# Kernel optimization log

Hardware: AMD Instinct MI355X
Metric: run time of the kernel (lower is better)

## Reference

```python
import jax, jax.numpy as jnp
import numpy as np

DIM = 256

def setup_inputs() -> dict:
    key = jax.random.key(0)
    k1, k2 = jax.random.split(key)
    X = jax.random.normal(k1, (4, 4096, DIM), dtype=jnp.float32)
    # fused QKV projection weight, stored as (dim, 3*dim) so y = X @ W + b
    W = jax.random.normal(k2, (DIM, 3 * DIM), dtype=jnp.float32) * (1.0 / np.sqrt(DIM))
    b = jnp.zeros((3 * DIM,), dtype=jnp.float32)
    return {"X": X, "W": W, "b": b}

def reference(X, W, b):
    dim = X.shape[-1]
    QKV = X @ W + b                      # [B, S, 3*dim]
    Q, K, V = jnp.split(QKV, 3, axis=-1)  # each [B, S, dim]
    scores = jnp.einsum('bqd,bkd->bqk', Q, K) / jnp.sqrt(jnp.float32(dim))
    weights = jax.nn.softmax(scores, axis=-1)  # [B, S, S]
    return jnp.einsum('bqk,bkd->bqd', weights, V)
```

## Files before the change

kernel.cpp:

```cpp
#include <hip/hip_runtime.h>
#include <hip/hip_bf16.h>
#include <hip/hip_fp16.h>

#define DIMD 256
#define SLEN 4096
#define KT 32

typedef __attribute__((ext_vector_type(8))) short short8;
typedef __attribute__((ext_vector_type(4))) short bf16x4;
typedef __attribute__((ext_vector_type(4))) float f32x4;
typedef unsigned int u32;

__device__ __forceinline__ ushort f2bf(float x) {
  union { float f; unsigned u; } v; v.f = x;
  unsigned r = v.u + 0x7fffu + ((v.u >> 16) & 1u);
  return (ushort)(r >> 16);
}

typedef __attribute__((address_space(1))) const u32 g_u32;
typedef __attribute__((address_space(3))) u32 l_u32;
__device__ __forceinline__ void gld_lds16(const void* g, void* l) {
  __builtin_amdgcn_global_load_lds((g_u32*)g, (l_u32*)l, 16, 0, 0);
}

__global__ __launch_bounds__(256) void wt_prep(const float* __restrict__ W,
                                               ushort* __restrict__ Wt) {
  __shared__ float T[32][257];
  const int t = threadIdx.x;
  const int n0 = blockIdx.x * 32;
#pragma unroll
  for (int pass = 0; pass < 8; ++pass) {
    const int k = pass * 32 + (t >> 3);
    const int c4 = (t & 7) * 4;
    const float4 f = *(const float4*)&W[(size_t)k * 768 + n0 + c4];
    T[c4 + 0][k] = f.x; T[c4 + 1][k] = f.y; T[c4 + 2][k] = f.z; T[c4 + 3][k] = f.w;
  }
  __syncthreads();
  const int n = t >> 3, kb = (t & 7) * 32;
#pragma unroll
  for (int j8 = 0; j8 < 4; ++j8) {
    short8 o;
#pragma unroll
    for (int j = 0; j < 8; ++j) o[j] = (short)f2bf(T[n][kb + j8 * 8 + j]);
    *(short8*)&Wt[(size_t)(n0 + n) * 256 + kb + j8 * 8] = o;
  }
}

__global__ __launch_bounds__(256, 2) void qkv_proj(const float* __restrict__ X,
                                                   const ushort* __restrict__ Wt,
                                                   const float* __restrict__ bias,
                                                   ushort* __restrict__ Qo,
                                                   ushort* __restrict__ Ko,
                                                   ushort* __restrict__ Vto) {
  __shared__ ushort Xs[128 * 36];
  __shared__ ushort Ws[256 * 36];
  const int tid = threadIdx.x;
  const int w = tid >> 6, lane = tid & 63;
  const int qa = lane & 15, hi = lane >> 4;
  const int m0 = blockIdx.x * 128;
  const int seg = blockIdx.y;
  const int n0 = seg * 256;

  f32x4 acc[2][16];
#pragma unroll
  for (int t = 0; t < 2; ++t)
#pragma unroll
    for (int dc = 0; dc < 16; ++dc) acc[t][dc] = (f32x4){0.f, 0.f, 0.f, 0.f};

  for (int k0 = 0; k0 < 256; k0 += 32) {
    __syncthreads();
#pragma unroll
    for (int pass = 0; pass < 4; ++pass) {
      const int row = pass * 32 + (tid >> 3);
      const int c = tid & 7;
      const float4 f = *(const float4*)&X[(size_t)(m0 + row) * 256 + k0 + c * 4];
      bf16x4 h = {(short)f2bf(f.x), (short)f2bf(f.y), (short)f2bf(f.z), (short)f2bf(f.w)};
      *(bf16x4*)&Xs[row * 36 + c * 4] = h;
    }
#pragma unroll
    for (int pass = 0; pass < 4; ++pass) {
      const int n = pass * 64 + (tid >> 2);
      const int c = (tid & 3) * 8;
      short8 v = *(const short8*)&Wt[(size_t)(n0 + n) * 256 + k0 + c];
      *(short8*)&Ws[n * 36 + c] = v;
    }
    __syncthreads();
    const short8 xf0 = *(const short8*)&Xs[(w * 32 + qa) * 36 + hi * 8];
    const short8 xf1 = *(const short8*)&Xs[(w * 32 + 16 + qa) * 36 + hi * 8];
    __builtin_amdgcn_s_setprio(1);
#pragma unroll
    for (int dc = 0; dc < 16; ++dc) {
      const short8 wf = *(const short8*)&Ws[(dc * 16 + qa) * 36 + hi * 8];
      acc[0][dc] = __builtin_amdgcn_mfma_f32_16x16x32_bf16(xf0, wf, acc[0][dc], 0, 0, 0);
      acc[1][dc] = __builtin_amdgcn_mfma_f32_16x16x32_bf16(xf1, wf, acc[1][dc], 0, 0, 0);
    }
    __builtin_amdgcn_s_setprio(0);
  }

  const float sc = (seg == 0) ? 0.0625f : 1.0f;
#pragma unroll
  for (int dc = 0; dc < 16; ++dc) {
    const int nn = dc * 16 + qa;
    const float bv = bias[n0 + nn];
#pragma unroll
    for (int t = 0; t < 2; ++t) {
#pragma unroll
      for (int r = 0; r < 4; ++r) {
        const int m = m0 + w * 32 + t * 16 + hi * 4 + r;
        const ushort h = f2bf((acc[t][dc][r] + bv) * sc);
        if (seg == 0)      Qo[(size_t)m * 256 + nn] = h;
        else if (seg == 1) Ko[(size_t)m * 256 + nn] = h;
        else {
          const int bi = m >> 12, s = m & 4095;
          const int sp = (s & ~31) | ((s & 3) | (((s >> 4) & 1) << 2) | (((s >> 2) & 3) << 3));
          Vto[((size_t)bi * 256 + nn) * 4096 + sp] = h;
        }
      }
    }
  }
}

__device__ __forceinline__ void stage_kv(ushort* KsB, ushort* VsB,
                                         const ushort* Kb, const ushort* Vtb,
                                         int kv0, int w, int lane) {
#pragma unroll
  for (int it = 0; it < 2; ++it) {
    const int row = w * 4 + it * 2 + (lane >> 5);
    const int cb = (lane & 31) * 16;
    const char* src = (const char*)Kb + (size_t)(kv0 + row) * 512 + (cb ^ ((row & 7) << 4));
    gld_lds16(src, (char*)KsB + w * 2048 + it * 1024);
  }
#pragma unroll
  for (int it = 0; it < 2; ++it) {
    const int d = w * 32 + it * 16 + (lane >> 2);
    const int cb = (lane & 3) * 16;
    const char* src = (const char*)Vtb + (size_t)d * 8192 + (size_t)kv0 * 2 + (cb ^ ((d & 3) << 4));
    gld_lds16(src, (char*)VsB + w * 2048 + it * 1024);
  }
}

__global__ __launch_bounds__(512, 2) void flash_attn(const ushort* __restrict__ Q,
                                                     const ushort* __restrict__ K,
                                                     const ushort* __restrict__ Vt,
                                                     float* __restrict__ Out,
                                                     __half* __restrict__ Op,
                                                     float* __restrict__ Mp,
                                                     int nsplit, int kvn) {
  __shared__ __attribute__((aligned(16))) ushort Ks[3][KT * DIMD];
  __shared__ __attribute__((aligned(16))) ushort Vs[3][DIMD * KT];

  const int tid = threadIdx.x;
  const int w = tid >> 6, lane = tid & 63;
  const int nwg = gridDim.x;
  const int wg = (blockIdx.x & 7) * (nwg >> 3) + (blockIdx.x >> 3);
  const int split = wg >> 6;
  const int rest = wg & 63;
  const int b = rest >> 4;
  const int q0 = (rest & 15) * 256;
  const int qa = lane & 15, hi = lane >> 4;

  const ushort* Qr0 = Q + (size_t)(b * SLEN + q0 + w * 32 + qa) * DIMD;
  short8 qf0[8], qf1[8];
#pragma unroll
  for (int dc = 0; dc < 8; ++dc) {
    qf0[dc] = *(const short8*)(Qr0 + dc * 32 + hi * 8);
    qf1[dc] = *(const short8*)(Qr0 + 16 * DIMD + dc * 32 + hi * 8);
  }

  const f32x4 zero = {0.f, 0.f, 0.f, 0.f};
  f32x4 acc[2][16];
#pragma unroll
  for (int t = 0; t < 2; ++t)
#pragma unroll
    for (int dc = 0; dc < 16; ++dc) acc[t][dc] = zero;
  float mold0 = -1e30f, lrun0 = 0.f, mold1 = -1e30f, lrun1 = 0.f;
  short8 af0, af1;

  const ushort* Kb = K + (size_t)b * SLEN * DIMD;
  const ushort* Vtb = Vt + (size_t)b * DIMD * SLEN;
  const int kv_begin = split * kvn;
  const int nt = kvn / KT;

  auto QK_SM = [&](const char* KsB) {
    f32x4 sa0 = zero, sa1 = zero, sb0 = zero, sb1 = zero;
    __builtin_amdgcn_s_setprio(1);
#pragma unroll
    for (int dc = 0; dc < 8; ++dc) {
      const int cb = dc * 64 + hi * 16;
      const short8 kf0 = *(const short8*)(KsB + ((qa * 512 + cb) ^ ((qa & 7) << 4)));
      const short8 kf1 = *(const short8*)(KsB + (((qa + 16) * 512 + cb) ^ ((qa & 7) << 4)));
      sa0 = __builtin_amdgcn_mfma_f32_16x16x32_bf16(kf0, qf0[dc], sa0, 0, 0, 0);
      sa1 = __builtin_amdgcn_mfma_f32_16x16x32_bf16(kf1, qf0[dc], sa1, 0, 0, 0);
      sb0 = __builtin_amdgcn_mfma_f32_16x16x32_bf16(kf0, qf1[dc], sb0, 0, 0, 0);
      sb1 = __builtin_amdgcn_mfma_f32_16x16x32_bf16(kf1, qf1[dc], sb1, 0, 0, 0);
    }
    __builtin_amdgcn_s_setprio(0);
    float m8a = fmaxf(fmaxf(fmaxf(sa0[0], sa0[1]), fmaxf(sa0[2], sa0[3])),
                      fmaxf(fmaxf(sa1[0], sa1[1]), fmaxf(sa1[2], sa1[3])));
    float m8b = fmaxf(fmaxf(fmaxf(sb0[0], sb0[1]), fmaxf(sb0[2], sb0[3])),
                      fmaxf(fmaxf(sb1[0], sb1[1]), fmaxf(sb1[2], sb1[3])));
    m8a = fmaxf(m8a, __shfl_xor(m8a, 16)); m8a = fmaxf(m8a, __shfl_xor(m8a, 32));
    m8b = fmaxf(m8b, __shfl_xor(m8b, 16)); m8b = fmaxf(m8b, __shfl_xor(m8b, 32));
    if (!__all(fmaxf(m8a - mold0, m8b - mold1) <= 4.0f)) {
      const float mn0 = fmaxf(mold0, m8a), fr0 = __expf(mold0 - mn0);
      const float mn1 = fmaxf(mold1, m8b), fr1 = __expf(mold1 - mn1);
      mold0 = mn0; lrun0 *= fr0; mold1 = mn1; lrun1 *= fr1;
      float fA[4], fB[4];
#pragma unroll
      for (int r = 0; r < 4; ++r) { fA[r] = __shfl(fr0, hi * 4 + r); fB[r] = __shfl(fr1, hi * 4 + r); }
#pragma unroll
      for (int dc = 0; dc < 16; ++dc)
#pragma unroll
        for (int r = 0; r < 4; ++r) { acc[0][dc][r] *= fA[r]; acc[1][dc][r] *= fB[r]; }
    }
    float ls0 = 0.f, ls1 = 0.f;
#pragma unroll
    for (int r = 0; r < 4; ++r) {
      float p = __expf(sa0[r] - mold0); ls0 += p; af0[r] = (short)f2bf(p);
      p = __expf(sa1[r] - mold0); ls0 += p; af0[4 + r] = (short)f2bf(p);
      p = __expf(sb0[r] - mold1); ls1 += p; af1[r] = (short)f2bf(p);
      p = __expf(sb1[r] - mold1); ls1 += p; af1[4 + r] = (short)f2bf(p);
    }
    ls0 += __shfl_xor(ls0, 16); ls0 += __shfl_xor(ls0, 32); lrun0 += ls0;
    ls1 += __shfl_xor(ls1, 16); ls1 += __shfl_xor(ls1, 32); lrun1 += ls1;
  };

  auto PV = [&](const char* VsB) {
    __builtin_amdgcn_s_setprio(1);
#pragma unroll
    for (int dc = 0; dc < 16; ++dc) {
      const int d = dc * 16 + qa;
      const short8 vf = *(const short8*)(VsB + d * 64 + ((hi * 16) ^ ((d & 3) << 4)));
      acc[0][dc] = __builtin_amdgcn_mfma_f32_16x16x32_bf16(af0, vf, acc[0][dc], 0, 0, 0);
      acc[1][dc] = __builtin_amdgcn_mfma_f32_16x16x32_bf16(af1, vf, acc[1][dc], 0, 0, 0);
    }
    __builtin_amdgcn_s_setprio(0);
  };

  stage_kv(Ks[0], Vs[0], Kb, Vtb, kv_begin, w, lane);
  stage_kv(Ks[1], Vs[1], Kb, Vtb, kv_begin + KT, w, lane);
  asm volatile("s_waitcnt vmcnt(4)" ::: "memory");
  __builtin_amdgcn_s_barrier();
  __builtin_amdgcn_sched_barrier(0);
  QK_SM((const char*)Ks[0]);

  int cur = 0;
  for (int it = 0; it < nt - 2; ++it) {
    const int nb = (cur == 0) ? 2 : cur - 1;
    stage_kv(Ks[nb], Vs[nb], Kb, Vtb, kv_begin + (it + 2) * KT, w, lane);
    __builtin_amdgcn_sched_barrier(0);
    PV((const char*)Vs[cur]);
    __builtin_amdgcn_sched_barrier(0);
    asm volatile("s_waitcnt vmcnt(4)" ::: "memory");
    const int nx = (cur == 2) ? 0 : cur + 1;
    QK_SM((const char*)Ks[nx]);
    __builtin_amdgcn_s_barrier();
    __builtin_amdgcn_sched_barrier(0);
    cur = nx;
  }
  PV((const char*)Vs[cur]);
  asm volatile("s_waitcnt vmcnt(0)" ::: "memory");
  __builtin_amdgcn_s_barrier();
  __builtin_amdgcn_sched_barrier(0);
  {
    const int nx = (cur == 2) ? 0 : cur + 1;
    QK_SM((const char*)Ks[nx]);
    PV((const char*)Vs[nx]);
  }

  float inv0[4], inv1[4];
#pragma unroll
  for (int r = 0; r < 4; ++r) {
    inv0[r] = 1.f / __shfl(lrun0, hi * 4 + r);
    inv1[r] = 1.f / __shfl(lrun1, hi * 4 + r);
  }
  if (nsplit == 1) {
    float* Ob = Out + (size_t)(b * SLEN + q0 + w * 32) * DIMD;
#pragma unroll
    for (int dc = 0; dc < 16; ++dc)
#pragma unroll
      for (int r = 0; r < 4; ++r) {
        Ob[(size_t)(hi * 4 + r) * DIMD + dc * 16 + qa] = acc[0][dc][r] * inv0[r];
        Ob[(size_t)(16 + hi * 4 + r) * DIMD + dc * 16 + qa] = acc[1][dc][r] * inv1[r];
      }
  } else {
    const size_t qrow0 = (size_t)b * SLEN + q0 + w * 32;
#pragma unroll
    for (int dc = 0; dc < 16; ++dc)
#pragma unroll
      for (int r = 0; r < 4; ++r) {
        Op[((qrow0 + hi * 4 + r) * nsplit + split) * DIMD + dc * 16 + qa] =
            __float2half(acc[0][dc][r] * inv0[r]);
        Op[((qrow0 + 16 + hi * 4 + r) * nsplit + split) * DIMD + dc * 16 + qa] =
            __float2half(acc[1][dc][r] * inv1[r]);
      }
    if (hi == 0) {
      Mp[(qrow0 + qa) * nsplit + split] = mold0 + __logf(lrun0);
      Mp[(qrow0 + 16 + qa) * nsplit + split] = mold1 + __logf(lrun1);
    }
  }
}

__global__ __launch_bounds__(256) void attn_merge(const __half* __restrict__ Op,
                                                  const float* __restrict__ Mp,
                                                  float* __restrict__ Out, int nsplit) {
  const int q = blockIdx.x, d = threadIdx.x;
  float Mx = -1e30f;
  for (int i = 0; i < nsplit; ++i) Mx = fmaxf(Mx, Mp[(size_t)q * nsplit + i]);
  float Wsum = 0.f, o = 0.f;
  for (int i = 0; i < nsplit; ++i) {
    const float wgt = __expf(Mp[(size_t)q * nsplit + i] - Mx);
    Wsum += wgt;
    o += wgt * __half2float(Op[((size_t)q * nsplit + i) * DIMD + d]);
  }
  Out[(size_t)q * DIMD + d] = o / Wsum;
}

extern "C" void kernel_launch(void* const* d_in, const int* in_sizes, int n_in,
                              void* d_out, int out_size, void* d_ws, size_t ws_size,
                              hipStream_t stream) {
  const float* X = (const float*)d_in[0];
  const float* W = (const float*)d_in[1];
  const float* bias = (const float*)d_in[2];
  char* wsb = (char*)d_ws;
  ushort* qw = (ushort*)wsb;
  ushort* kw = qw + (size_t)16384 * 256;
  ushort* vtw = kw + (size_t)16384 * 256;
  ushort* wt = vtw + (size_t)16384 * 256;
  const size_t head_bytes = (size_t)3 * 16384 * 256 * 2 + 768 * 256 * 2;
  const size_t per_split = (size_t)16384 * 256 * 2 + (size_t)16384 * 4;
  int nsplit = 1;
  if (ws_size >= head_bytes + 4 * per_split)      nsplit = 4;
  else if (ws_size >= head_bytes + 2 * per_split) nsplit = 2;
  __half* Op = (__half*)(wsb + head_bytes);
  float* Mp = (float*)(wsb + head_bytes + (size_t)nsplit * 16384 * 256 * 2);

  wt_prep<<<dim3(24), 256, 0, stream>>>(W, wt);
  qkv_proj<<<dim3(128, 3), 256, 0, stream>>>(X, wt, bias, qw, kw, vtw);
  flash_attn<<<dim3(64 * nsplit), 512, 0, stream>>>(qw, kw, vtw, (float*)d_out,
                                                    Op, Mp, nsplit, 4096 / nsplit);
  if (nsplit > 1)
    attn_merge<<<dim3(16384), 256, 0, stream>>>(Op, Mp, (float*)d_out, nsplit);
}
```

Measured before the change: 142.2 us.

## Interleave PV and next-tile QK MFMAs and defer softmax row reductions

```diff
diff --git a/kernel.cpp b/kernel.cpp
--- a/kernel.cpp
+++ b/kernel.cpp
@@ -175,14 +175,15 @@
     for (int dc = 0; dc < 16; ++dc) acc[t][dc] = zero;
   float mold0 = -1e30f, lrun0 = 0.f, mold1 = -1e30f, lrun1 = 0.f;
   short8 af0, af1;
+  f32x4 sa0, sa1, sb0, sb1;
 
   const ushort* Kb = K + (size_t)b * SLEN * DIMD;
   const ushort* Vtb = Vt + (size_t)b * DIMD * SLEN;
   const int kv_begin = split * kvn;
   const int nt = kvn / KT;
 
-  auto QK_SM = [&](const char* KsB) {
-    f32x4 sa0 = zero, sa1 = zero, sb0 = zero, sb1 = zero;
+  auto QK = [&](const char* KsB) {
+    sa0 = zero; sa1 = zero; sb0 = zero; sb1 = zero;
     __builtin_amdgcn_s_setprio(1);
 #pragma unroll
     for (int dc = 0; dc < 8; ++dc) {
@@ -195,13 +196,40 @@
       sb1 = __builtin_amdgcn_mfma_f32_16x16x32_bf16(kf1, qf1[dc], sb1, 0, 0, 0);
     }
     __builtin_amdgcn_s_setprio(0);
+  };
+
+  auto FUSED = [&](const char* VsB, const char* KsB) {
+    sa0 = zero; sa1 = zero; sb0 = zero; sb1 = zero;
+    __builtin_amdgcn_s_setprio(1);
+#pragma unroll
+    for (int j = 0; j < 8; ++j) {
+      const int d0 = (2 * j) * 16 + qa;
+      const short8 vfa = *(const short8*)(VsB + d0 * 64 + ((hi * 16) ^ ((d0 & 3) << 4)));
+      acc[0][2 * j] = __builtin_amdgcn_mfma_f32_16x16x32_bf16(af0, vfa, acc[0][2 * j], 0, 0, 0);
+      acc[1][2 * j] = __builtin_amdgcn_mfma_f32_16x16x32_bf16(af1, vfa, acc[1][2 * j], 0, 0, 0);
+      const int d1 = d0 + 16;
+      const short8 vfb = *(const short8*)(VsB + d1 * 64 + ((hi * 16) ^ ((d1 & 3) << 4)));
+      acc[0][2 * j + 1] = __builtin_amdgcn_mfma_f32_16x16x32_bf16(af0, vfb, acc[0][2 * j + 1], 0, 0, 0);
+      acc[1][2 * j + 1] = __builtin_amdgcn_mfma_f32_16x16x32_bf16(af1, vfb, acc[1][2 * j + 1], 0, 0, 0);
+      const int cb = j * 64 + hi * 16;
+      const short8 kf0 = *(const short8*)(KsB + ((qa * 512 + cb) ^ ((qa & 7) << 4)));
+      const short8 kf1 = *(const short8*)(KsB + (((qa + 16) * 512 + cb) ^ ((qa & 7) << 4)));
+      sa0 = __builtin_amdgcn_mfma_f32_16x16x32_bf16(kf0, qf0[j], sa0, 0, 0, 0);
+      sa1 = __builtin_amdgcn_mfma_f32_16x16x32_bf16(kf1, qf0[j], sa1, 0, 0, 0);
+      sb0 = __builtin_amdgcn_mfma_f32_16x16x32_bf16(kf0, qf1[j], sb0, 0, 0, 0);
+      sb1 = __builtin_amdgcn_mfma_f32_16x16x32_bf16(kf1, qf1[j], sb1, 0, 0, 0);
+    }
+    __builtin_amdgcn_s_setprio(0);
+  };
+
+  auto SM = [&]() {
     float m8a = fmaxf(fmaxf(fmaxf(sa0[0], sa0[1]), fmaxf(sa0[2], sa0[3])),
                       fmaxf(fmaxf(sa1[0], sa1[1]), fmaxf(sa1[2], sa1[3])));
     float m8b = fmaxf(fmaxf(fmaxf(sb0[0], sb0[1]), fmaxf(sb0[2], sb0[3])),
                       fmaxf(fmaxf(sb1[0], sb1[1]), fmaxf(sb1[2], sb1[3])));
-    m8a = fmaxf(m8a, __shfl_xor(m8a, 16)); m8a = fmaxf(m8a, __shfl_xor(m8a, 32));
-    m8b = fmaxf(m8b, __shfl_xor(m8b, 16)); m8b = fmaxf(m8b, __shfl_xor(m8b, 32));
     if (!__all(fmaxf(m8a - mold0, m8b - mold1) <= 4.0f)) {
+      m8a = fmaxf(m8a, __shfl_xor(m8a, 16)); m8a = fmaxf(m8a, __shfl_xor(m8a, 32));
+      m8b = fmaxf(m8b, __shfl_xor(m8b, 16)); m8b = fmaxf(m8b, __shfl_xor(m8b, 32));
       const float mn0 = fmaxf(mold0, m8a), fr0 = __expf(mold0 - mn0);
       const float mn1 = fmaxf(mold1, m8b), fr1 = __expf(mold1 - mn1);
       mold0 = mn0; lrun0 *= fr0; mold1 = mn1; lrun1 *= fr1;
@@ -221,8 +249,8 @@
       p = __expf(sb0[r] - mold1); ls1 += p; af1[r] = (short)f2bf(p);
       p = __expf(sb1[r] - mold1); ls1 += p; af1[4 + r] = (short)f2bf(p);
     }
-    ls0 += __shfl_xor(ls0, 16); ls0 += __shfl_xor(ls0, 32); lrun0 += ls0;
-    ls1 += __shfl_xor(ls1, 16); ls1 += __shfl_xor(ls1, 32); lrun1 += ls1;
+    lrun0 += ls0;
+    lrun1 += ls1;
   };
 
   auto PV = [&](const char* VsB) {
@@ -239,35 +267,38 @@
 
   stage_kv(Ks[0], Vs[0], Kb, Vtb, kv_begin, w, lane);
   stage_kv(Ks[1], Vs[1], Kb, Vtb, kv_begin + KT, w, lane);
-  asm volatile("s_waitcnt vmcnt(4)" ::: "memory");
+  asm volatile("s_waitcnt vmcnt(0)" ::: "memory");
   __builtin_amdgcn_s_barrier();
   __builtin_amdgcn_sched_barrier(0);
-  QK_SM((const char*)Ks[0]);
+  QK((const char*)Ks[0]);
+  SM();
 
   int cur = 0;
   for (int it = 0; it < nt - 2; ++it) {
     const int nb = (cur == 0) ? 2 : cur - 1;
     stage_kv(Ks[nb], Vs[nb], Kb, Vtb, kv_begin + (it + 2) * KT, w, lane);
     __builtin_amdgcn_sched_barrier(0);
-    PV((const char*)Vs[cur]);
+    asm volatile("s_waitcnt vmcnt(4)" ::: "memory");
     __builtin_amdgcn_sched_barrier(0);
-    asm volatile("s_waitcnt vmcnt(4)" ::: "memory");
     const int nx = (cur == 2) ? 0 : cur + 1;
-    QK_SM((const char*)Ks[nx]);
+    FUSED((const char*)Vs[cur], (const char*)Ks[nx]);
+    SM();
     __builtin_amdgcn_s_barrier();
     __builtin_amdgcn_sched_barrier(0);
     cur = nx;
   }
-  PV((const char*)Vs[cur]);
   asm volatile("s_waitcnt vmcnt(0)" ::: "memory");
   __builtin_amdgcn_s_barrier();
   __builtin_amdgcn_sched_barrier(0);
   {
     const int nx = (cur == 2) ? 0 : cur + 1;
-    QK_SM((const char*)Ks[nx]);
+    FUSED((const char*)Vs[cur], (const char*)Ks[nx]);
+    SM();
     PV((const char*)Vs[nx]);
   }
 
+  lrun0 += __shfl_xor(lrun0, 16); lrun0 += __shfl_xor(lrun0, 32);
+  lrun1 += __shfl_xor(lrun1, 16); lrun1 += __shfl_xor(lrun1, 32);
   float inv0[4], inv1[4];
 #pragma unroll
   for (int r = 0; r < 4; ++r) {
```

New measurement: 142.4 us. Within noise of the previous version (+0.1%).
